# Performance work log

Measured on AMD Instinct MI355X. Metric: run time of the kernel, lower is better.

The kernel has to match this reference:

```python
import jax, jax.numpy as jnp
import numpy as np

DIM = 512
NUM_HEADS = 8
HEAD_DIM = DIM // NUM_HEADS
SCALE = HEAD_DIM ** -0.5


def setup_inputs() -> dict:
    key = jax.random.key(0)
    ks = jax.random.split(key, 10)
    B, Sq, Skv = 4, 2048, 2048
    std = DIM ** -0.5
    return {
        "x1": jax.random.normal(ks[0], (B, Sq, DIM), jnp.float32),
        "x2": jax.random.normal(ks[1], (B, Skv, DIM), jnp.float32),
        "Wq": jax.random.normal(ks[2], (DIM, DIM), jnp.float32) * std,
        "bq": jax.random.normal(ks[3], (DIM,), jnp.float32) * 0.02,
        "Wk": jax.random.normal(ks[4], (DIM, DIM), jnp.float32) * std,
        "bk": jax.random.normal(ks[5], (DIM,), jnp.float32) * 0.02,
        "Wv": jax.random.normal(ks[6], (DIM, DIM), jnp.float32) * std,
        "bv": jax.random.normal(ks[7], (DIM,), jnp.float32) * 0.02,
        "Wo": jax.random.normal(ks[8], (DIM, DIM), jnp.float32) * std,
        "bo": jax.random.normal(ks[9], (DIM,), jnp.float32) * 0.02,
    }


def reference(x1, x2, Wq, bq, Wk, bk, Wv, bv, Wo, bo):
    B, Sq, _ = x1.shape
    Skv = x2.shape[1]
    # Linear projections (torch nn.Linear: x @ W.T + b)
    Q = (x1 @ Wq.T + bq).reshape(B, Sq, NUM_HEADS, HEAD_DIM)
    K = (x2 @ Wk.T + bk).reshape(B, Skv, NUM_HEADS, HEAD_DIM)
    V = (x2 @ Wv.T + bv).reshape(B, Skv, NUM_HEADS, HEAD_DIM)
    # [B, H, Sq, Skv]
    attn = jnp.einsum("bqhd,bkhd->bhqk", Q, K) * SCALE
    attn = jax.nn.softmax(attn, axis=-1)  # dropout is identity in eval mode
    out = jnp.einsum("bhqk,bkhd->bqhd", attn, V).reshape(B, Sq, DIM)
    return out @ Wo.T + bo
```

## Files before the change

### kernel.cpp

```cpp
#include <hip/hip_runtime.h>
#include <math.h>

constexpr int kB = 4, kS = 2048, kDim = 512, kNH = 8, kHD = 64;
constexpr float kQScale = 0.18033688011112042f;

using bf16x8 = __attribute__((ext_vector_type(8))) short;
using f32x4  = __attribute__((ext_vector_type(4))) float;

__device__ __forceinline__ unsigned pack_rn(float f0, float f1) {
  unsigned a = __builtin_bit_cast(unsigned, f0) + 0x8000u;
  unsigned b = __builtin_bit_cast(unsigned, f1) + 0x8000u;
  return __builtin_amdgcn_perm(b, a, 0x07060302u);
}
__device__ __forceinline__ float fexp2(float x) {
#if __has_builtin(__builtin_amdgcn_exp2f)
  return __builtin_amdgcn_exp2f(x);
#else
  return exp2f(x);
#endif
}

#define GLDS(gp, lp) __builtin_amdgcn_global_load_lds(                         \
    (const __attribute__((address_space(1))) void*)(gp),                       \
    (__attribute__((address_space(3))) void*)(lp), 16, 0, 0)

__global__ __launch_bounds__(256) void cvt_bf16(
    const float* __restrict__ x1, const float* __restrict__ x2,
    const float* __restrict__ Wq, const float* __restrict__ Wk,
    const float* __restrict__ Wv, const float* __restrict__ Wo,
    unsigned short* __restrict__ x1b, unsigned short* __restrict__ x2b,
    unsigned short* __restrict__ wb) {
  const size_t i = (size_t)blockIdx.x * 256 + threadIdx.x;
  const float* src;
  unsigned short* dst;
  size_t off;
  if (i < 1048576) { src = x1; dst = x1b; off = i; }
  else if (i < 2097152) { src = x2; dst = x2b; off = i - 1048576; }
  else {
    const size_t j = i - 2097152;
    const int seg = (int)(j >> 16);
    src = seg == 0 ? Wq : seg == 1 ? Wk : seg == 2 ? Wv : Wo;
    dst = wb + (size_t)seg * 262144;
    off = j & 65535;
  }
  const float4 v = *(const float4*)(src + off * 4);
  uint2 o;
  o.x = pack_rn(v.x, v.y);
  o.y = pack_rn(v.z, v.w);
  *(uint2*)(dst + off * 4) = o;
}

__global__ __launch_bounds__(256) void qkv_gemm(
    const unsigned short* __restrict__ x1b, const unsigned short* __restrict__ x2b,
    const unsigned short* __restrict__ wb,
    const float* __restrict__ bq, const float* __restrict__ bk,
    const float* __restrict__ bv,
    unsigned short* __restrict__ Qg, unsigned short* __restrict__ Kg,
    unsigned short* __restrict__ Vg) {
  __shared__ __align__(16) short As0[2][128 * 32], As1[2][128 * 32];
  __shared__ __align__(16) short Bs0[2][64 * 32], Bs1[2][64 * 32];
  const int z = blockIdx.z;
  const unsigned short* X = z ? x2b : x1b;
  const unsigned short* W = wb + (size_t)z * (kDim * kDim);
  const float* bias = (z == 0) ? bq : (z == 1) ? bk : bv;

  const int t = threadIdx.x, lane = t & 63, w = t >> 6;
  const int g = lane >> 4, c = lane & 15;
  const int bm = blockIdx.y * 128, bn = blockIdx.x * 64;
  const int lr = lane >> 2, lc = (lane & 3) * 8;

#pragma unroll
  for (int i = 0; i < 2; ++i) {
    const int row = i * 64 + w * 16;
    const size_t ga = (size_t)(bm + row + lr) * kDim + lc;
    GLDS(X + ga, &As0[0][row * 32]);
    GLDS(X + ga + 32, &As1[0][row * 32]);
  }
  {
    const int row = w * 16;
    const size_t gb = (size_t)(bn + row + lr) * kDim + lc;
    GLDS(W + gb, &Bs0[0][row * 32]);
    GLDS(W + gb + 32, &Bs1[0][row * 32]);
  }
  __syncthreads();

  f32x4 acc[8] = {};
  int ib = 0;
  for (int k0 = 0; k0 < kDim; k0 += 64, ib ^= 1) {
    if (k0 + 64 < kDim) {
      const int nb = ib ^ 1;
#pragma unroll
      for (int i = 0; i < 2; ++i) {
        const int row = i * 64 + w * 16;
        const size_t ga = (size_t)(bm + row + lr) * kDim + k0 + 64 + lc;
        GLDS(X + ga, &As0[nb][row * 32]);
        GLDS(X + ga + 32, &As1[nb][row * 32]);
      }
      {
        const int row = w * 16;
        const size_t gb = (size_t)(bn + row + lr) * kDim + k0 + 64 + lc;
        GLDS(W + gb, &Bs0[nb][row * 32]);
        GLDS(W + gb + 32, &Bs1[nb][row * 32]);
      }
    }
#pragma unroll
    for (int kk = 0; kk < 2; ++kk) {
      const short* Ap = kk ? As1[ib] : As0[ib];
      const short* Bp = kk ? Bs1[ib] : Bs0[ib];
      if (z == 2) {
        bf16x8 fa[2], fb[4];
#pragma unroll
        for (int i = 0; i < 2; ++i) fa[i] = *(const bf16x8*)&Ap[(w * 32 + i * 16 + c) * 32 + g * 8];
#pragma unroll
        for (int j = 0; j < 4; ++j) fb[j] = *(const bf16x8*)&Bp[(j * 16 + c) * 32 + g * 8];
#pragma unroll
        for (int i = 0; i < 2; ++i)
#pragma unroll
          for (int j = 0; j < 4; ++j)
            acc[i * 4 + j] = __builtin_amdgcn_mfma_f32_16x16x32_bf16(fa[i], fb[j], acc[i * 4 + j], 0, 0, 0);
      } else {
        bf16x8 fa[4], fb[2];
#pragma unroll
        for (int i = 0; i < 4; ++i) fa[i] = *(const bf16x8*)&Bp[(i * 16 + c) * 32 + g * 8];
#pragma unroll
        for (int j = 0; j < 2; ++j) fb[j] = *(const bf16x8*)&Ap[(w * 32 + j * 16 + c) * 32 + g * 8];
#pragma unroll
        for (int i = 0; i < 4; ++i)
#pragma unroll
          for (int j = 0; j < 2; ++j)
            acc[i * 2 + j] = __builtin_amdgcn_mfma_f32_16x16x32_bf16(fa[i], fb[j], acc[i * 2 + j], 0, 0, 0);
      }
    }
    __syncthreads();
  }

  if (z == 2) {
    const int h_ = bn >> 6;
#pragma unroll
    for (int i = 0; i < 2; ++i)
#pragma unroll
      for (int j = 0; j < 4; ++j) {
        const int n = bn + j * 16 + c;
        const float bb = bias[n];
        const int m0 = bm + w * 32 + i * 16 + g * 4;
        const int b_ = m0 >> 11, s0 = m0 & 2047;
        const int d_ = n & 63;
        const f32x4 a = acc[i * 4 + j];
        uint2 pv;
        pv.x = pack_rn(a[0] + bb, a[1] + bb);
        pv.y = pack_rn(a[2] + bb, a[3] + bb);
        *(uint2*)(Vg + (((size_t)((b_ * kNH + h_) * kHD + d_)) << 11) + s0) = pv;
      }
  } else {
    const float sc = (z == 0) ? kQScale : 1.0f;
    unsigned short* Og = z ? Kg : Qg;
    const int h_ = bn >> 6;
#pragma unroll
    for (int i = 0; i < 4; ++i) {
      const int n0 = bn + i * 16 + g * 4;
      const float4 bb = *(const float4*)(bias + n0);
      const int d0 = n0 & 63;
#pragma unroll
      for (int j = 0; j < 2; ++j) {
        const int m = bm + w * 32 + j * 16 + c;
        const int b_ = m >> 11, s_ = m & 2047;
        const f32x4 a = acc[i * 2 + j];
        uint2 st;
        st.x = pack_rn((a[0] + bb.x) * sc, (a[1] + bb.y) * sc);
        st.y = pack_rn((a[2] + bb.z) * sc, (a[3] + bb.w) * sc);
        *(uint2*)(Og + (((size_t)((b_ * kNH + h_) * kS + s_)) << 6) + d0) = st;
      }
    }
  }
}

__global__ __launch_bounds__(256) void out_gemm(const unsigned short* __restrict__ A,
                                                const unsigned short* __restrict__ Wob,
                                                const float* __restrict__ bias,
                                                float* __restrict__ Y) {
  __shared__ __align__(16) short As0[2][64 * 32], As1[2][64 * 32];
  __shared__ __align__(16) short Bs0[2][64 * 32], Bs1[2][64 * 32];
  const int t = threadIdx.x, lane = t & 63, w = t >> 6;
  const int g = lane >> 4, c = lane & 15;
  const int bm = blockIdx.y * 64, bn = blockIdx.x * 64;
  const int wm = (w >> 1) * 32, wn = (w & 1) * 32;
  const int lr = lane >> 2, lc = (lane & 3) * 8;

  {
    const int row = w * 16;
    const size_t ga = (size_t)(bm + row + lr) * kDim + lc;
    const size_t gb = (size_t)(bn + row + lr) * kDim + lc;
    GLDS(A + ga, &As0[0][row * 32]);
    GLDS(A + ga + 32, &As1[0][row * 32]);
    GLDS(Wob + gb, &Bs0[0][row * 32]);
    GLDS(Wob + gb + 32, &Bs1[0][row * 32]);
  }
  __syncthreads();

  f32x4 acc[2][2] = {};
  int ib = 0;
  for (int k0 = 0; k0 < kDim; k0 += 64, ib ^= 1) {
    if (k0 + 64 < kDim) {
      const int nb = ib ^ 1;
      const int row = w * 16;
      const size_t ga = (size_t)(bm + row + lr) * kDim + k0 + 64 + lc;
      const size_t gb = (size_t)(bn + row + lr) * kDim + k0 + 64 + lc;
      GLDS(A + ga, &As0[nb][row * 32]);
      GLDS(A + ga + 32, &As1[nb][row * 32]);
      GLDS(Wob + gb, &Bs0[nb][row * 32]);
      GLDS(Wob + gb + 32, &Bs1[nb][row * 32]);
    }
#pragma unroll
    for (int kk = 0; kk < 2; ++kk) {
      const short* Ap = kk ? As1[ib] : As0[ib];
      const short* Bp = kk ? Bs1[ib] : Bs0[ib];
      bf16x8 fa[2], fb[2];
#pragma unroll
      for (int i = 0; i < 2; ++i) fa[i] = *(const bf16x8*)&Bp[(wn + i * 16 + c) * 32 + g * 8];
#pragma unroll
      for (int j = 0; j < 2; ++j) fb[j] = *(const bf16x8*)&Ap[(wm + j * 16 + c) * 32 + g * 8];
#pragma unroll
      for (int i = 0; i < 2; ++i)
#pragma unroll
        for (int j = 0; j < 2; ++j)
          acc[i][j] = __builtin_amdgcn_mfma_f32_16x16x32_bf16(fa[i], fb[j], acc[i][j], 0, 0, 0);
    }
    __syncthreads();
  }
#pragma unroll
  for (int i = 0; i < 2; ++i) {
    const int n0 = bn + wn + i * 16 + g * 4;
    const float4 bb = *(const float4*)(bias + n0);
#pragma unroll
    for (int j = 0; j < 2; ++j) {
      const int m = bm + wm + j * 16 + c;
      float4 st;
      st.x = acc[i][j][0] + bb.x;
      st.y = acc[i][j][1] + bb.y;
      st.z = acc[i][j][2] + bb.z;
      st.w = acc[i][j][3] + bb.w;
      *(float4*)(Y + (size_t)m * kDim + n0) = st;
    }
  }
}

__global__ __launch_bounds__(256, 2) void flash_mfma(const unsigned short* __restrict__ Qg,
                                                     const unsigned short* __restrict__ Kg,
                                                     const unsigned short* __restrict__ Vg,
                                                     unsigned short* __restrict__ attn) {
  __shared__ __align__(16) short Ks[64 * 76];
  __shared__ __align__(16) short Vs[64 * 76];
  const int t = threadIdx.x, lane = t & 63, w = t >> 6;
  const int c = lane & 15, g4 = lane >> 4;
  const int bh = blockIdx.x, q0 = blockIdx.y * 128;
  const int b_ = bh >> 3, h_ = bh & 7;

  const unsigned short* Qp = Qg + ((size_t)bh * kS + q0) * kHD;
  const unsigned short* Kp = Kg + (size_t)bh * kS * kHD;
  const unsigned short* Vp = Vg + (size_t)bh * kHD * kS;

  bf16x8 bq[2][2];
  {
    const unsigned short* qr = Qp + (size_t)(w * 32 + c) * kHD + g4 * 8;
    bq[0][0] = *(const bf16x8*)qr;
    bq[1][0] = *(const bf16x8*)(qr + 32);
    bq[0][1] = *(const bf16x8*)(qr + 16 * kHD);
    bq[1][1] = *(const bf16x8*)(qr + 16 * kHD + 32);
  }

  const int r0 = t >> 3, cc0 = (t & 7) * 8;
  const int ps = (((r0 >> 2) & 1) << 4) | (((r0 >> 3) & 3) << 2) | (r0 & 3);
  const unsigned short* kpt = Kp + (size_t)r0 * kHD + cc0;
  const unsigned short* vpt = Vp + (size_t)r0 * kS + cc0;
  uint4 pk0 = *(const uint4*)kpt;
  uint4 pk1 = *(const uint4*)(kpt + 32 * kHD);
  uint4 pv0 = *(const uint4*)vpt;
  uint4 pv1 = *(const uint4*)(vpt + 32 * kS);
  kpt += 64 * kHD;
  vpt += 64;

  float l[2] = {0.f, 0.f};
  f32x4 o[4][2] = {};

  for (int kv0 = 0; kv0 < kS; kv0 += 64) {
    __syncthreads();
    *(uint4*)&Ks[ps * 76 + cc0] = pk0;
    *(uint4*)&Ks[(ps + 32) * 76 + cc0] = pk1;
    *(uint4*)&Vs[r0 * 76 + cc0] = pv0;
    *(uint4*)&Vs[(r0 + 32) * 76 + cc0] = pv1;
    if (kv0 + 64 < kS) {
      pk0 = *(const uint4*)kpt;
      pk1 = *(const uint4*)(kpt + 32 * kHD);
      pv0 = *(const uint4*)vpt;
      pv1 = *(const uint4*)(vpt + 32 * kS);
      kpt += 64 * kHD;
      vpt += 64;
    }
    __syncthreads();

    f32x4 sa[4][2] = {};
#pragma unroll
    for (int ks = 0; ks < 2; ++ks)
#pragma unroll
      for (int kt = 0; kt < 4; ++kt) {
        const bf16x8 a = *(const bf16x8*)&Ks[(kt * 16 + c) * 76 + ks * 32 + g4 * 8];
        sa[kt][0] = __builtin_amdgcn_mfma_f32_16x16x32_bf16(a, bq[ks][0], sa[kt][0], 0, 0, 0);
        sa[kt][1] = __builtin_amdgcn_mfma_f32_16x16x32_bf16(a, bq[ks][1], sa[kt][1], 0, 0, 0);
      }

#pragma unroll
    for (int ks = 0; ks < 2; ++ks) {
      bf16x8 bpf[2];
#pragma unroll
      for (int qs = 0; qs < 2; ++qs) {
        const float p0 = fexp2(sa[2 * ks][qs][0]), p1 = fexp2(sa[2 * ks][qs][1]);
        const float p2 = fexp2(sa[2 * ks][qs][2]), p3 = fexp2(sa[2 * ks][qs][3]);
        const float p4 = fexp2(sa[2 * ks + 1][qs][0]), p5 = fexp2(sa[2 * ks + 1][qs][1]);
        const float p6 = fexp2(sa[2 * ks + 1][qs][2]), p7 = fexp2(sa[2 * ks + 1][qs][3]);
        l[qs] += ((p0 + p1) + (p2 + p3)) + ((p4 + p5) + (p6 + p7));
        uint4 bp;
        bp.x = pack_rn(p0, p1);
        bp.y = pack_rn(p2, p3);
        bp.z = pack_rn(p4, p5);
        bp.w = pack_rn(p6, p7);
        bpf[qs] = __builtin_bit_cast(bf16x8, bp);
      }
#pragma unroll
      for (int dt = 0; dt < 4; ++dt) {
        const bf16x8 va = *(const bf16x8*)&Vs[(dt * 16 + c) * 76 + ks * 32 + g4 * 8];
        o[dt][0] = __builtin_amdgcn_mfma_f32_16x16x32_bf16(va, bpf[0], o[dt][0], 0, 0, 0);
        o[dt][1] = __builtin_amdgcn_mfma_f32_16x16x32_bf16(va, bpf[1], o[dt][1], 0, 0, 0);
      }
    }
  }

#pragma unroll
  for (int qs = 0; qs < 2; ++qs) {
    l[qs] += __shfl_xor(l[qs], 16, 64);
    l[qs] += __shfl_xor(l[qs], 32, 64);
  }
#pragma unroll
  for (int qs = 0; qs < 2; ++qs) {
    const float inv = 1.0f / l[qs];
    unsigned short* orow =
        attn + ((size_t)(b_ * kS + q0 + w * 32 + qs * 16 + c)) * kDim + h_ * kHD;
#pragma unroll
    for (int dt = 0; dt < 4; ++dt) {
      uint2 st;
      st.x = pack_rn(o[dt][qs][0] * inv, o[dt][qs][1] * inv);
      st.y = pack_rn(o[dt][qs][2] * inv, o[dt][qs][3] * inv);
      *(uint2*)(orow + dt * 16 + g4 * 4) = st;
    }
  }
}

extern "C" void kernel_launch(void* const* d_in, const int* in_sizes, int n_in,
                              void* d_out, int out_size, void* d_ws, size_t ws_size,
                              hipStream_t stream) {
  const float* x1 = (const float*)d_in[0];
  const float* x2 = (const float*)d_in[1];
  const float* Wq = (const float*)d_in[2];
  const float* bq = (const float*)d_in[3];
  const float* Wk = (const float*)d_in[4];
  const float* bk = (const float*)d_in[5];
  const float* Wv = (const float*)d_in[6];
  const float* bv = (const float*)d_in[7];
  const float* Wo = (const float*)d_in[8];
  const float* bo = (const float*)d_in[9];
  float* out = (float*)d_out;

  constexpr size_t kTok = (size_t)kB * kS * kDim;
  unsigned short* x1b = (unsigned short*)d_ws;
  unsigned short* x2b = x1b + kTok;
  unsigned short* wb  = x2b + kTok;
  unsigned short* Qg  = wb + 4 * (size_t)(kDim * kDim);
  unsigned short* Kg  = Qg + kTok;
  unsigned short* Vg  = Kg + kTok;
  unsigned short* atb = Vg + kTok;

  const dim3 blk(256);
  cvt_bf16<<<dim3(9216), blk, 0, stream>>>(x1, x2, Wq, Wk, Wv, Wo, x1b, x2b, wb);
  qkv_gemm<<<dim3(8, 64, 3), blk, 0, stream>>>(x1b, x2b, wb, bq, bk, bv, Qg, Kg, Vg);
  flash_mfma<<<dim3(32, 16), blk, 0, stream>>>(Qg, Kg, Vg, atb);
  out_gemm<<<dim3(8, 128), blk, 0, stream>>>(atb, wb + 3 * (size_t)(kDim * kDim), bo, out);
}
```

Before: 191.6 us.

## Enlarge GEMM tiles with swizzled LDS and double-buffer K/V in flash attention

Both projection GEMMs move to 128x128 block tiles with a 2x2 warp grid, 64-wide K slabs and an XOR-swizzled LDS layout, so each block reuses more operand data and LDS reads avoid bank conflicts. Launch grids shrink to match the larger tiles. The flash attention kernel double-buffers its K/V shared tiles, dropping one barrier per iteration, and raises wave priority around the MFMA sections with s_setprio. The larger tiles use more LDS and registers per block and give fewer blocks, which may lower occupancy or leave CUs underused.

```diff
diff --git a/kernel.cpp b/kernel.cpp
--- a/kernel.cpp
+++ b/kernel.cpp
@@ -50,15 +50,15 @@
   *(uint2*)(dst + off * 4) = o;
 }
 
-__global__ __launch_bounds__(256) void qkv_gemm(
+__global__ __launch_bounds__(256, 2) void qkv_gemm(
     const unsigned short* __restrict__ x1b, const unsigned short* __restrict__ x2b,
     const unsigned short* __restrict__ wb,
     const float* __restrict__ bq, const float* __restrict__ bk,
     const float* __restrict__ bv,
     unsigned short* __restrict__ Qg, unsigned short* __restrict__ Kg,
     unsigned short* __restrict__ Vg) {
-  __shared__ __align__(16) short As0[2][128 * 32], As1[2][128 * 32];
-  __shared__ __align__(16) short Bs0[2][64 * 32], Bs1[2][64 * 32];
+  __shared__ __align__(16) short As[2][128 * 64];
+  __shared__ __align__(16) short Bs[2][128 * 64];
   const int z = blockIdx.z;
   const unsigned short* X = z ? x2b : x1b;
   const unsigned short* W = wb + (size_t)z * (kDim * kDim);
@@ -66,83 +66,72 @@
 
   const int t = threadIdx.x, lane = t & 63, w = t >> 6;
   const int g = lane >> 4, c = lane & 15;
-  const int bm = blockIdx.y * 128, bn = blockIdx.x * 64;
-  const int lr = lane >> 2, lc = (lane & 3) * 8;
-
-#pragma unroll
-  for (int i = 0; i < 2; ++i) {
-    const int row = i * 64 + w * 16;
-    const size_t ga = (size_t)(bm + row + lr) * kDim + lc;
-    GLDS(X + ga, &As0[0][row * 32]);
-    GLDS(X + ga + 32, &As1[0][row * 32]);
-  }
-  {
-    const int row = w * 16;
-    const size_t gb = (size_t)(bn + row + lr) * kDim + lc;
-    GLDS(W + gb, &Bs0[0][row * 32]);
-    GLDS(W + gb + 32, &Bs1[0][row * 32]);
+  const int bm = blockIdx.y * 128, bn = blockIdx.x * 128;
+  const int wm = (w >> 1) * 64, wn = (w & 1) * 64;
+
+  const int srow = lane >> 3;
+  const int schunk = ((lane & 7) ^ srow) * 8;
+  const int wrow = w * 32;
+
+#pragma unroll
+  for (int i8 = 0; i8 < 4; ++i8) {
+    const int row = wrow + i8 * 8;
+    GLDS(X + (size_t)(bm + row + srow) * kDim + schunk, &As[0][row * 64]);
+    GLDS(W + (size_t)(bn + row + srow) * kDim + schunk, &Bs[0][row * 64]);
   }
   __syncthreads();
 
-  f32x4 acc[8] = {};
+  f32x4 acc[16] = {};
   int ib = 0;
   for (int k0 = 0; k0 < kDim; k0 += 64, ib ^= 1) {
     if (k0 + 64 < kDim) {
       const int nb = ib ^ 1;
 #pragma unroll
-      for (int i = 0; i < 2; ++i) {
-        const int row = i * 64 + w * 16;
-        const size_t ga = (size_t)(bm + row + lr) * kDim + k0 + 64 + lc;
-        GLDS(X + ga, &As0[nb][row * 32]);
-        GLDS(X + ga + 32, &As1[nb][row * 32]);
-      }
-      {
-        const int row = w * 16;
-        const size_t gb = (size_t)(bn + row + lr) * kDim + k0 + 64 + lc;
-        GLDS(W + gb, &Bs0[nb][row * 32]);
-        GLDS(W + gb + 32, &Bs1[nb][row * 32]);
+      for (int i8 = 0; i8 < 4; ++i8) {
+        const int row = wrow + i8 * 8;
+        GLDS(X + (size_t)(bm + row + srow) * kDim + k0 + 64 + schunk, &As[nb][row * 64]);
+        GLDS(W + (size_t)(bn + row + srow) * kDim + k0 + 64 + schunk, &Bs[nb][row * 64]);
       }
     }
 #pragma unroll
     for (int kk = 0; kk < 2; ++kk) {
-      const short* Ap = kk ? As1[ib] : As0[ib];
-      const short* Bp = kk ? Bs1[ib] : Bs0[ib];
+      const int sx = ((kk * 4 + g) ^ (c & 7)) * 8;
       if (z == 2) {
-        bf16x8 fa[2], fb[4];
-#pragma unroll
-        for (int i = 0; i < 2; ++i) fa[i] = *(const bf16x8*)&Ap[(w * 32 + i * 16 + c) * 32 + g * 8];
-#pragma unroll
-        for (int j = 0; j < 4; ++j) fb[j] = *(const bf16x8*)&Bp[(j * 16 + c) * 32 + g * 8];
-#pragma unroll
-        for (int i = 0; i < 2; ++i)
+        bf16x8 fa[4], fb[4];
+#pragma unroll
+        for (int i = 0; i < 4; ++i) fa[i] = *(const bf16x8*)&As[ib][(wm + i * 16 + c) * 64 + sx];
+#pragma unroll
+        for (int j = 0; j < 4; ++j) fb[j] = *(const bf16x8*)&Bs[ib][(wn + j * 16 + c) * 64 + sx];
+#pragma unroll
+        for (int i = 0; i < 4; ++i)
 #pragma unroll
           for (int j = 0; j < 4; ++j)
             acc[i * 4 + j] = __builtin_amdgcn_mfma_f32_16x16x32_bf16(fa[i], fb[j], acc[i * 4 + j], 0, 0, 0);
       } else {
-        bf16x8 fa[4], fb[2];
-#pragma unroll
-        for (int i = 0; i < 4; ++i) fa[i] = *(const bf16x8*)&Bp[(i * 16 + c) * 32 + g * 8];
-#pragma unroll
-        for (int j = 0; j < 2; ++j) fb[j] = *(const bf16x8*)&Ap[(w * 32 + j * 16 + c) * 32 + g * 8];
+        bf16x8 fa[4], fb[4];
+#pragma unroll
+        for (int i = 0; i < 4; ++i) fa[i] = *(const bf16x8*)&Bs[ib][(wn + i * 16 + c) * 64 + sx];
+#pragma unroll
+        for (int j = 0; j < 4; ++j) fb[j] = *(const bf16x8*)&As[ib][(wm + j * 16 + c) * 64 + sx];
 #pragma unroll
         for (int i = 0; i < 4; ++i)
 #pragma unroll
-          for (int j = 0; j < 2; ++j)
-            acc[i * 2 + j] = __builtin_amdgcn_mfma_f32_16x16x32_bf16(fa[i], fb[j], acc[i * 2 + j], 0, 0, 0);
+          for (int j = 0; j < 4; ++j)
+            acc[i * 4 + j] = __builtin_amdgcn_mfma_f32_16x16x32_bf16(fa[i], fb[j], acc[i * 4 + j], 0, 0, 0);
       }
     }
     __syncthreads();
   }
 
   if (z == 2) {
-    const int h_ = bn >> 6;
-#pragma unroll
-    for (int i = 0; i < 2; ++i)
+    const int h_ = (bn + wn) >> 6;
+#pragma unroll
+    for (int i = 0; i < 4; ++i)
 #pragma unroll
       for (int j = 0; j < 4; ++j) {
-        const int n = bn + j * 16 + c;
+        const int n = bn + wn + j * 16 + c;
         const float bb = bias[n];
-        const int m0 = bm + w * 32 + i * 16 + g * 4;
+        const int m0 = bm + wm + i * 16 + g * 4;
         const int b_ = m0 >> 11, s0 = m0 & 2047;
         const int d_ = n & 63;
         const f32x4 a = acc[i * 4 + j];
@@ -154,17 +143,17 @@
   } else {
     const float sc = (z == 0) ? kQScale : 1.0f;
     unsigned short* Og = z ? Kg : Qg;
-    const int h_ = bn >> 6;
+    const int h_ = (bn + wn) >> 6;
 #pragma unroll
     for (int i = 0; i < 4; ++i) {
-      const int n0 = bn + i * 16 + g * 4;
+      const int n0 = bn + wn + i * 16 + g * 4;
       const float4 bb = *(const float4*)(bias + n0);
       const int d0 = n0 & 63;
 #pragma unroll
-      for (int j = 0; j < 2; ++j) {
-        const int m = bm + w * 32 + j * 16 + c;
+      for (int j = 0; j < 4; ++j) {
+        const int m = bm + wm + j * 16 + c;
         const int b_ = m >> 11, s_ = m & 2047;
-        const f32x4 a = acc[i * 2 + j];
+        const f32x4 a = acc[i * 4 + j];
         uint2 st;
         st.x = pack_rn((a[0] + bb.x) * sc, (a[1] + bb.y) * sc);
         st.y = pack_rn((a[2] + bb.z) * sc, (a[3] + bb.w) * sc);
@@ -174,71 +163,69 @@
   }
 }
 
-__global__ __launch_bounds__(256) void out_gemm(const unsigned short* __restrict__ A,
-                                                const unsigned short* __restrict__ Wob,
-                                                const float* __restrict__ bias,
-                                                float* __restrict__ Y) {
-  __shared__ __align__(16) short As0[2][64 * 32], As1[2][64 * 32];
-  __shared__ __align__(16) short Bs0[2][64 * 32], Bs1[2][64 * 32];
+__global__ __launch_bounds__(256, 2) void out_gemm(const unsigned short* __restrict__ A,
+                                                   const unsigned short* __restrict__ Wob,
+                                                   const float* __restrict__ bias,
+                                                   float* __restrict__ Y) {
+  __shared__ __align__(16) short As[2][128 * 64];
+  __shared__ __align__(16) short Bs[2][128 * 64];
   const int t = threadIdx.x, lane = t & 63, w = t >> 6;
   const int g = lane >> 4, c = lane & 15;
-  const int bm = blockIdx.y * 64, bn = blockIdx.x * 64;
-  const int wm = (w >> 1) * 32, wn = (w & 1) * 32;
-  const int lr = lane >> 2, lc = (lane & 3) * 8;
-
-  {
-    const int row = w * 16;
-    const size_t ga = (size_t)(bm + row + lr) * kDim + lc;
-    const size_t gb = (size_t)(bn + row + lr) * kDim + lc;
-    GLDS(A + ga, &As0[0][row * 32]);
-    GLDS(A + ga + 32, &As1[0][row * 32]);
-    GLDS(Wob + gb, &Bs0[0][row * 32]);
-    GLDS(Wob + gb + 32, &Bs1[0][row * 32]);
+  const int bm = blockIdx.y * 128, bn = blockIdx.x * 128;
+  const int wm = (w >> 1) * 64, wn = (w & 1) * 64;
+  const int srow = lane >> 3;
+  const int schunk = ((lane & 7) ^ srow) * 8;
+  const int wrow = w * 32;
+
+#pragma unroll
+  for (int i8 = 0; i8 < 4; ++i8) {
+    const int row = wrow + i8 * 8;
+    GLDS(A + (size_t)(bm + row + srow) * kDim + schunk, &As[0][row * 64]);
+    GLDS(Wob + (size_t)(bn + row + srow) * kDim + schunk, &Bs[0][row * 64]);
   }
   __syncthreads();
 
-  f32x4 acc[2][2] = {};
+  f32x4 acc[16] = {};
   int ib = 0;
   for (int k0 = 0; k0 < kDim; k0 += 64, ib ^= 1) {
     if (k0 + 64 < kDim) {
       const int nb = ib ^ 1;
-      const int row = w * 16;
-      const size_t ga = (size_t)(bm + row + lr) * kDim + k0 + 64 + lc;
-      const size_t gb = (size_t)(bn + row + lr) * kDim + k0 + 64 + lc;
-      GLDS(A + ga, &As0[nb][row * 32]);
-      GLDS(A + ga + 32, &As1[nb][row * 32]);
-      GLDS(Wob + gb, &Bs0[nb][row * 32]);
-      GLDS(Wob + gb + 32, &Bs1[nb][row * 32]);
+#pragma unroll
+      for (int i8 = 0; i8 < 4; ++i8) {
+        const int row = wrow + i8 * 8;
+        GLDS(A + (size_t)(bm + row + srow) * kDim + k0 + 64 + schunk, &As[nb][row * 64]);
+        GLDS(Wob + (size_t)(bn + row + srow) * kDim + k0 + 64 + schunk, &Bs[nb][row * 64]);
+      }
     }
 #pragma unroll
     for (int kk = 0; kk < 2; ++kk) {
-      const short* Ap = kk ? As1[ib] : As0[ib];
-      const short* Bp = kk ? Bs1[ib] : Bs0[ib];
-      bf16x8 fa[2], fb[2];
-#pragma unroll
-      for (int i = 0; i < 2; ++i) fa[i] = *(const bf16x8*)&Bp[(wn + i * 16 + c) * 32 + g * 8];
-#pragma unroll
-      for (int j = 0; j < 2; ++j) fb[j] = *(const bf16x8*)&Ap[(wm + j * 16 + c) * 32 + g * 8];
-#pragma unroll
-      for (int i = 0; i < 2; ++i)
-#pragma unroll
-        for (int j = 0; j < 2; ++j)
-          acc[i][j] = __builtin_amdgcn_mfma_f32_16x16x32_bf16(fa[i], fb[j], acc[i][j], 0, 0, 0);
+      const int sx = ((kk * 4 + g) ^ (c & 7)) * 8;
+      bf16x8 fa[4], fb[4];
+#pragma unroll
+      for (int i = 0; i < 4; ++i) fa[i] = *(const bf16x8*)&Bs[ib][(wn + i * 16 + c) * 64 + sx];
+#pragma unroll
+      for (int j = 0; j < 4; ++j) fb[j] = *(const bf16x8*)&As[ib][(wm + j * 16 + c) * 64 + sx];
+#pragma unroll
+      for (int i = 0; i < 4; ++i)
+#pragma unroll
+        for (int j = 0; j < 4; ++j)
+          acc[i * 4 + j] = __builtin_amdgcn_mfma_f32_16x16x32_bf16(fa[i], fb[j], acc[i * 4 + j], 0, 0, 0);
     }
     __syncthreads();
   }
 #pragma unroll
-  for (int i = 0; i < 2; ++i) {
+  for (int i = 0; i < 4; ++i) {
     const int n0 = bn + wn + i * 16 + g * 4;
     const float4 bb = *(const float4*)(bias + n0);
 #pragma unroll
-    for (int j = 0; j < 2; ++j) {
+    for (int j = 0; j < 4; ++j) {
       const int m = bm + wm + j * 16 + c;
+      const f32x4 a = acc[i * 4 + j];
       float4 st;
-      st.x = acc[i][j][0] + bb.x;
-      st.y = acc[i][j][1] + bb.y;
-      st.z = acc[i][j][2] + bb.z;
-      st.w = acc[i][j][3] + bb.w;
+      st.x = a[0] + bb.x;
+      st.y = a[1] + bb.y;
+      st.z = a[2] + bb.z;
+      st.w = a[3] + bb.w;
       *(float4*)(Y + (size_t)m * kDim + n0) = st;
     }
   }
@@ -248,8 +235,8 @@
                                                      const unsigned short* __restrict__ Kg,
                                                      const unsigned short* __restrict__ Vg,
                                                      unsigned short* __restrict__ attn) {
-  __shared__ __align__(16) short Ks[64 * 76];
-  __shared__ __align__(16) short Vs[64 * 76];
+  __shared__ __align__(16) short Ks[2][64 * 76];
+  __shared__ __align__(16) short Vs[2][64 * 76];
   const int t = threadIdx.x, lane = t & 63, w = t >> 6;
   const int c = lane & 15, g4 = lane >> 4;
   const int bh = blockIdx.x, q0 = blockIdx.y * 128;
@@ -272,23 +259,41 @@
   const int ps = (((r0 >> 2) & 1) << 4) | (((r0 >> 3) & 3) << 2) | (r0 & 3);
   const unsigned short* kpt = Kp + (size_t)r0 * kHD + cc0;
   const unsigned short* vpt = Vp + (size_t)r0 * kS + cc0;
+
   uint4 pk0 = *(const uint4*)kpt;
   uint4 pk1 = *(const uint4*)(kpt + 32 * kHD);
   uint4 pv0 = *(const uint4*)vpt;
   uint4 pv1 = *(const uint4*)(vpt + 32 * kS);
   kpt += 64 * kHD;
   vpt += 64;
+  *(uint4*)&Ks[0][ps * 76 + cc0] = pk0;
+  *(uint4*)&Ks[0][(ps + 32) * 76 + cc0] = pk1;
+  *(uint4*)&Vs[0][r0 * 76 + cc0] = pv0;
+  *(uint4*)&Vs[0][(r0 + 32) * 76 + cc0] = pv1;
+  pk0 = *(const uint4*)kpt;
+  pk1 = *(const uint4*)(kpt + 32 * kHD);
+  pv0 = *(const uint4*)vpt;
+  pv1 = *(const uint4*)(vpt + 32 * kS);
+  kpt += 64 * kHD;
+  vpt += 64;
+  __syncthreads();
 
   float l[2] = {0.f, 0.f};
   f32x4 o[4][2] = {};
 
-  for (int kv0 = 0; kv0 < kS; kv0 += 64) {
-    __syncthreads();
-    *(uint4*)&Ks[ps * 76 + cc0] = pk0;
-    *(uint4*)&Ks[(ps + 32) * 76 + cc0] = pk1;
-    *(uint4*)&Vs[r0 * 76 + cc0] = pv0;
-    *(uint4*)&Vs[(r0 + 32) * 76 + cc0] = pv1;
-    if (kv0 + 64 < kS) {
+  for (int it = 0; it < kS / 64; ++it) {
+    const int b = it & 1;
+    const short* Kb = Ks[b];
+    const short* Vb = Vs[b];
+    if (it < kS / 64 - 1) {
+      short* Kn = Ks[b ^ 1];
+      short* Vn = Vs[b ^ 1];
+      *(uint4*)&Kn[ps * 76 + cc0] = pk0;
+      *(uint4*)&Kn[(ps + 32) * 76 + cc0] = pk1;
+      *(uint4*)&Vn[r0 * 76 + cc0] = pv0;
+      *(uint4*)&Vn[(r0 + 32) * 76 + cc0] = pv1;
+    }
+    if (it < kS / 64 - 2) {
       pk0 = *(const uint4*)kpt;
       pk1 = *(const uint4*)(kpt + 32 * kHD);
       pv0 = *(const uint4*)vpt;
@@ -296,17 +301,18 @@
       kpt += 64 * kHD;
       vpt += 64;
     }
-    __syncthreads();
 
     f32x4 sa[4][2] = {};
+    __builtin_amdgcn_s_setprio(1);
 #pragma unroll
     for (int ks = 0; ks < 2; ++ks)
 #pragma unroll
       for (int kt = 0; kt < 4; ++kt) {
-        const bf16x8 a = *(const bf16x8*)&Ks[(kt * 16 + c) * 76 + ks * 32 + g4 * 8];
+        const bf16x8 a = *(const bf16x8*)&Kb[(kt * 16 + c) * 76 + ks * 32 + g4 * 8];
         sa[kt][0] = __builtin_amdgcn_mfma_f32_16x16x32_bf16(a, bq[ks][0], sa[kt][0], 0, 0, 0);
         sa[kt][1] = __builtin_amdgcn_mfma_f32_16x16x32_bf16(a, bq[ks][1], sa[kt][1], 0, 0, 0);
       }
+    __builtin_amdgcn_s_setprio(0);
 
 #pragma unroll
     for (int ks = 0; ks < 2; ++ks) {
@@ -325,13 +331,16 @@
         bp.w = pack_rn(p6, p7);
         bpf[qs] = __builtin_bit_cast(bf16x8, bp);
       }
+      __builtin_amdgcn_s_setprio(1);
 #pragma unroll
       for (int dt = 0; dt < 4; ++dt) {
-        const bf16x8 va = *(const bf16x8*)&Vs[(dt * 16 + c) * 76 + ks * 32 + g4 * 8];
+        const bf16x8 va = *(const bf16x8*)&Vb[(dt * 16 + c) * 76 + ks * 32 + g4 * 8];
         o[dt][0] = __builtin_amdgcn_mfma_f32_16x16x32_bf16(va, bpf[0], o[dt][0], 0, 0, 0);
         o[dt][1] = __builtin_amdgcn_mfma_f32_16x16x32_bf16(va, bpf[1], o[dt][1], 0, 0, 0);
       }
-    }
+      __builtin_amdgcn_s_setprio(0);
+    }
+    if (it < kS / 64 - 1) __syncthreads();
   }
 
 #pragma unroll
@@ -380,7 +389,7 @@
 
   const dim3 blk(256);
   cvt_bf16<<<dim3(9216), blk, 0, stream>>>(x1, x2, Wq, Wk, Wv, Wo, x1b, x2b, wb);
-  qkv_gemm<<<dim3(8, 64, 3), blk, 0, stream>>>(x1b, x2b, wb, bq, bk, bv, Qg, Kg, Vg);
+  qkv_gemm<<<dim3(4, 64, 3), blk, 0, stream>>>(x1b, x2b, wb, bq, bk, bv, Qg, Kg, Vg);
   flash_mfma<<<dim3(32, 16), blk, 0, stream>>>(Qg, Kg, Vg, atb);
-  out_gemm<<<dim3(8, 128), blk, 0, stream>>>(atb, wb + 3 * (size_t)(kDim * kDim), bo, out);
-}
+  out_gemm<<<dim3(4, 64), blk, 0, stream>>>(atb, wb + 3 * (size_t)(kDim * kDim), bo, out);
+}
```

Measured after the change: 270.1 us. +41.0%, slower.
